# Kernel optimization log

Measured on AMD Instinct MI355X. Metric: run time of the kernel, lower is better.

## Reference

```python
import jax, jax.numpy as jnp
import numpy as np

EQUATION = "bik,bkj->bij"  # matches init_kwargs


def setup_inputs() -> dict:
    key = jax.random.key(0)
    k0, k1 = jax.random.split(key)
    B, I, K, J = 32, 2048, 128, 2048
    input_0 = jax.random.normal(k0, (B, I, K), dtype=jnp.float32)
    input_1 = jax.random.normal(k1, (B, K, J), dtype=jnp.float32)
    return {"input_0": input_0, "input_1": input_1}


def reference(input_0, input_1):
    # Einsum module forward: binary contraction per the stored equation,
    # alpha=1, beta=0 (defaults in EinsumFunction when kwargs is empty).
    return jnp.einsum(EQUATION, input_0, input_1)
```

## Files before the change

kernel.cpp:

```cpp
#include <hip/hip_runtime.h>
#include <hip/hip_bf16.h>
#include <stdint.h>

#define B_DIM 32
#define I_DIM 2048
#define J_DIM 2048
#define K_DIM 128

typedef __attribute__((ext_vector_type(8))) short bf16x8;
typedef __attribute__((ext_vector_type(4))) short short4v;
typedef __attribute__((ext_vector_type(4))) float f32x4;

__device__ inline short f2bf(float f) {
  union { float f; uint32_t u; } v; v.f = f;
  uint32_t u = v.u + 0x7fffu + ((v.u >> 16) & 1u);
  return (short)(u >> 16);
}

__global__ __launch_bounds__(256) void convA_kernel(const float* __restrict__ A,
                                                    short* __restrict__ Ab) {
  const int idx = blockIdx.x * 256 + threadIdx.x;
  const float4* p = reinterpret_cast<const float4*>(A) + (size_t)idx * 2;
  const float4 a = p[0], b = p[1];
  bf16x8 o;
  o[0] = f2bf(a.x); o[1] = f2bf(a.y); o[2] = f2bf(a.z); o[3] = f2bf(a.w);
  o[4] = f2bf(b.x); o[5] = f2bf(b.y); o[6] = f2bf(b.z); o[7] = f2bf(b.w);
  reinterpret_cast<bf16x8*>(Ab)[idx] = o;
}

__global__ __launch_bounds__(256) void transB_kernel(const float* __restrict__ B,
                                                     short* __restrict__ Bt) {
  __shared__ __align__(16) short tile[64 * 128];
  const int t  = threadIdx.x;
  const int j0 = blockIdx.x * 64;
  const int b  = blockIdx.y;
  const float* Bb = B + (size_t)b * K_DIM * J_DIM;
  const int jj = t & 63, kq = t >> 6;
  #pragma unroll
  for (int kr = 0; kr < 32; ++kr) {
    const int k = kr * 4 + kq;
    const float v = Bb[(size_t)k * J_DIM + j0 + jj];
    tile[jj * 128 + (k ^ ((jj & 15) << 3))] = f2bf(v);
  }
  __syncthreads();
  short* Btb = Bt + (size_t)b * J_DIM * K_DIM;
  const int slot = t & 15, jr = t >> 4;
  #pragma unroll
  for (int r2 = 0; r2 < 4; ++r2) {
    const int j  = r2 * 16 + jr;
    const bf16x8 v = *reinterpret_cast<const bf16x8*>(&tile[j * 128 + slot * 8]);
    const int k0 = (slot * 8) ^ ((j & 15) << 3);
    *reinterpret_cast<bf16x8*>(Btb + (size_t)(j0 + j) * K_DIM + k0) = v;
  }
}

#define GLD_LDS16(g, l) __builtin_amdgcn_global_load_lds( \
    (const __attribute__((address_space(1))) uint32_t*)(g), \
    (__attribute__((address_space(3))) uint32_t*)(l), 16, 0, 0)

__global__ __launch_bounds__(256, 4) void gemm_kernel(const short* __restrict__ Ab,
                                                      const short* __restrict__ Bt,
                                                      float* __restrict__ C) {
  __shared__ __align__(16) short As[8192];
  __shared__ __align__(16) short Bs[8192];
  const int t  = threadIdx.x;
  const int jt = blockIdx.x, it = blockIdx.y, b = blockIdx.z;

  const int rsub  = t >> 3;
  const int kbyte = ((t & 7) << 4) ^ ((rsub & 7) << 4);
  const char* Asrc = (const char*)(Ab + (size_t)(b * I_DIM + it * 128 + rsub) * K_DIM) + kbyte;
  const char* Bsrc = (const char*)(Bt + (size_t)(b * J_DIM + jt * 128 + rsub) * K_DIM) + kbyte;
  char* Adst = (char*)As + (t >> 6) * 1024;
  char* Bdst = (char*)Bs + (t >> 6) * 1024;

  const int w = t >> 6, wm = w >> 1, wn = w & 1;
  const int lane = t & 63, lr = lane & 15, g = lane >> 4;
  const int swr = (lr & 7) << 4;

  f32x4 acc[4][4];
  #pragma unroll
  for (int m = 0; m < 4; ++m)
    #pragma unroll
    for (int n = 0; n < 4; ++n)
      acc[m][n] = (f32x4){0.f, 0.f, 0.f, 0.f};

  #pragma unroll
  for (int ki = 0; ki < 2; ++ki) {
    if (ki) __syncthreads();
    #pragma unroll
    for (int q = 0; q < 4; ++q) {
      GLD_LDS16(Asrc + q * 8192 + ki * 128, Adst + q * 4096);
      GLD_LDS16(Bsrc + q * 8192 + ki * 128, Bdst + q * 4096);
    }
    __syncthreads();
    #pragma unroll
    for (int kk = 0; kk < 2; ++kk) {
      bf16x8 af[4], bb[4];
      const int cb = kk * 64 + g * 16;
      #pragma unroll
      for (int m = 0; m < 4; ++m) {
        const int R = wm * 64 + m * 16 + lr;
        af[m] = *reinterpret_cast<const bf16x8*>((const char*)As + R * 128 + (cb ^ swr));
      }
      #pragma unroll
      for (int n = 0; n < 4; ++n) {
        const int R = wn * 64 + n * 16 + lr;
        bb[n] = *reinterpret_cast<const bf16x8*>((const char*)Bs + R * 128 + (cb ^ swr));
      }
      #pragma unroll
      for (int m = 0; m < 4; ++m)
        #pragma unroll
        for (int n = 0; n < 4; ++n)
          acc[m][n] = __builtin_amdgcn_mfma_f32_16x16x32_bf16(af[m], bb[n], acc[m][n], 0, 0, 0);
    }
  }

  float* Cb = C + (size_t)b * I_DIM * J_DIM;
  const int cbase = jt * 128 + wn * 64 + lr;
  #pragma unroll
  for (int m = 0; m < 4; ++m) {
    const int rbase = it * 128 + wm * 64 + m * 16 + g * 4;
    #pragma unroll
    for (int q = 0; q < 4; ++q) {
      float* crow = Cb + (size_t)(rbase + q) * J_DIM + cbase;
      #pragma unroll
      for (int n = 0; n < 4; ++n) crow[n * 16] = acc[m][n][q];
    }
  }
}

__device__ inline int swz_fb(int row, int kbyte) {
  return row * 128 + ((kbyte ^ ((row & 15) << 4)) >> 1);
}

__global__ __launch_bounds__(256, 2) void bmm_fallback(const float* __restrict__ A,
                                                       const float* __restrict__ Bm,
                                                       float* __restrict__ C) {
  __shared__ short As[128 * 128];
  __shared__ short Bs[128 * 128];
  const int t  = threadIdx.x;
  const int jt = blockIdx.x, it = blockIdx.y, b = blockIdx.z;
  const float* Abp = A  + (size_t)b * I_DIM * K_DIM;
  const float* Bbp = Bm + (size_t)b * K_DIM * J_DIM;
  {
    const int r0 = t >> 5;
    const int k0 = (t & 31) * 4;
    #pragma unroll 4
    for (int i8 = 0; i8 < 16; ++i8) {
      const int r = i8 * 8 + r0;
      const float4 v = *reinterpret_cast<const float4*>(
          Abp + (size_t)(it * 128 + r) * K_DIM + k0);
      short4v s; s.x = f2bf(v.x); s.y = f2bf(v.y); s.z = f2bf(v.z); s.w = f2bf(v.w);
      *reinterpret_cast<short4v*>(&As[swz_fb(r, 2 * k0)]) = s;
    }
  }
  {
    const int j  = t & 127;
    const int kq = (t >> 7) * 4;
    #pragma unroll 4
    for (int kb = 0; kb < 16; ++kb) {
      const int k0 = kb * 8 + kq;
      const float* p = Bbp + (size_t)k0 * J_DIM + jt * 128 + j;
      const float f0 = p[0], f1 = p[J_DIM], f2 = p[2 * J_DIM], f3 = p[3 * J_DIM];
      short4v s; s.x = f2bf(f0); s.y = f2bf(f1); s.z = f2bf(f2); s.w = f2bf(f3);
      *reinterpret_cast<short4v*>(&Bs[swz_fb(j, 2 * k0)]) = s;
    }
  }
  __syncthreads();
  const int w = t >> 6, wm = w >> 1, wn = w & 1;
  const int lane = t & 63, lr = lane & 15, g = lane >> 4;
  f32x4 acc[4][4];
  #pragma unroll
  for (int m = 0; m < 4; ++m)
    #pragma unroll
    for (int n = 0; n < 4; ++n) acc[m][n] = (f32x4){0.f, 0.f, 0.f, 0.f};
  #pragma unroll
  for (int kk = 0; kk < 4; ++kk) {
    bf16x8 af[4], bfr[4];
    const int kb = kk * 64 + g * 16;
    #pragma unroll
    for (int m = 0; m < 4; ++m) {
      const int r = wm * 64 + m * 16 + lr;
      af[m] = *reinterpret_cast<const bf16x8*>(&As[swz_fb(r, kb)]);
    }
    #pragma unroll
    for (int n = 0; n < 4; ++n) {
      const int r = wn * 64 + n * 16 + lr;
      bfr[n] = *reinterpret_cast<const bf16x8*>(&Bs[swz_fb(r, kb)]);
    }
    #pragma unroll
    for (int m = 0; m < 4; ++m)
      #pragma unroll
      for (int n = 0; n < 4; ++n)
        acc[m][n] = __builtin_amdgcn_mfma_f32_16x16x32_bf16(af[m], bfr[n], acc[m][n], 0, 0, 0);
  }
  float* Cb = C + (size_t)b * I_DIM * J_DIM;
  const int cbase = jt * 128 + wn * 64 + lr;
  #pragma unroll
  for (int m = 0; m < 4; ++m) {
    const int rbase = it * 128 + wm * 64 + m * 16 + g * 4;
    #pragma unroll
    for (int q = 0; q < 4; ++q) {
      float* crow = Cb + (size_t)(rbase + q) * J_DIM + cbase;
      #pragma unroll
      for (int n = 0; n < 4; ++n) crow[n * 16] = acc[m][n][q];
    }
  }
}

extern "C" void kernel_launch(void* const* d_in, const int* in_sizes, int n_in,
                              void* d_out, int out_size, void* d_ws, size_t ws_size,
                              hipStream_t stream) {
  const float* A  = (const float*)d_in[0];
  const float* Bm = (const float*)d_in[1];
  float* C = (float*)d_out;
  const size_t needA = (size_t)B_DIM * I_DIM * K_DIM * sizeof(short);
  const size_t needB = (size_t)B_DIM * K_DIM * J_DIM * sizeof(short);
  if (ws_size >= needA + needB) {
    short* Ab = (short*)d_ws;
    short* Bt = (short*)((char*)d_ws + needA);
    convA_kernel<<<4096, 256, 0, stream>>>(A, Ab);
    transB_kernel<<<dim3(J_DIM / 64, B_DIM), 256, 0, stream>>>(Bm, Bt);
    gemm_kernel<<<dim3(J_DIM / 128, I_DIM / 128, B_DIM), 256, 0, stream>>>(Ab, Bt, C);
  } else {
    bmm_fallback<<<dim3(J_DIM / 128, I_DIM / 128, B_DIM), 256, 0, stream>>>(A, Bm, C);
  }
}
```

Measured before the change: 147.7 us.

## Restructure GEMM into single-wave 64x64 tiles with barrier-free LDS prefetch

Replaces the 256-thread 128x128 tile GEMM with a 64-thread, single-wavefront kernel that computes a 64x64 tile. Because only one wave uses the LDS, workgroup barriers are replaced by explicit waitcnt and sched_barrier fencing. The second K-half is loaded into the same LDS buffer once the first half's fragments are in registers, so it overlaps the remaining MFMAs. A 1D grid with a blockIdx remap interleaves batches and tiles across dispatch. The cost is less data reuse per tile, which roughly doubles global and LDS reads of A and B per output element, plus many more small workgroups.

```diff
diff --git a/kernel.cpp b/kernel.cpp
--- a/kernel.cpp
+++ b/kernel.cpp
@@ -58,24 +58,24 @@
     (const __attribute__((address_space(1))) uint32_t*)(g), \
     (__attribute__((address_space(3))) uint32_t*)(l), 16, 0, 0)
 
-__global__ __launch_bounds__(256, 4) void gemm_kernel(const short* __restrict__ Ab,
-                                                      const short* __restrict__ Bt,
-                                                      float* __restrict__ C) {
-  __shared__ __align__(16) short As[8192];
-  __shared__ __align__(16) short Bs[8192];
-  const int t  = threadIdx.x;
-  const int jt = blockIdx.x, it = blockIdx.y, b = blockIdx.z;
-
-  const int rsub  = t >> 3;
-  const int kbyte = ((t & 7) << 4) ^ ((rsub & 7) << 4);
-  const char* Asrc = (const char*)(Ab + (size_t)(b * I_DIM + it * 128 + rsub) * K_DIM) + kbyte;
-  const char* Bsrc = (const char*)(Bt + (size_t)(b * J_DIM + jt * 128 + rsub) * K_DIM) + kbyte;
-  char* Adst = (char*)As + (t >> 6) * 1024;
-  char* Bdst = (char*)Bs + (t >> 6) * 1024;
-
-  const int w = t >> 6, wm = w >> 1, wn = w & 1;
-  const int lane = t & 63, lr = lane & 15, g = lane >> 4;
-  const int swr = (lr & 7) << 4;
+__global__ __launch_bounds__(64, 4) void gemm_kernel(const short* __restrict__ Ab,
+                                                     const short* __restrict__ Bt,
+                                                     float* __restrict__ C) {
+  __shared__ __align__(16) char lds[16384];
+  const int l = threadIdx.x;
+
+  const int p   = blockIdx.x;
+  const int lid = ((p & 7) << 12) | (p >> 3);
+  const int jt  = lid & 31;
+  const int it  = (lid >> 5) & 31;
+  const int b   = lid >> 10;
+
+  const int rs = l >> 3;
+  const int cs = ((l & 7) ^ rs) << 4;
+  const char* Ag = (const char*)(Ab + ((size_t)b * I_DIM + it * 64 + rs) * K_DIM) + cs;
+  const char* Bg = (const char*)(Bt + ((size_t)b * J_DIM + jt * 64 + rs) * K_DIM) + cs;
+
+  const int lr = l & 15, g = l >> 4;
 
   f32x4 acc[4][4];
   #pragma unroll
@@ -85,41 +85,59 @@
       acc[m][n] = (f32x4){0.f, 0.f, 0.f, 0.f};
 
   #pragma unroll
-  for (int ki = 0; ki < 2; ++ki) {
-    if (ki) __syncthreads();
-    #pragma unroll
-    for (int q = 0; q < 4; ++q) {
-      GLD_LDS16(Asrc + q * 8192 + ki * 128, Adst + q * 4096);
-      GLD_LDS16(Bsrc + q * 8192 + ki * 128, Bdst + q * 4096);
-    }
-    __syncthreads();
-    #pragma unroll
-    for (int kk = 0; kk < 2; ++kk) {
-      bf16x8 af[4], bb[4];
-      const int cb = kk * 64 + g * 16;
-      #pragma unroll
-      for (int m = 0; m < 4; ++m) {
-        const int R = wm * 64 + m * 16 + lr;
-        af[m] = *reinterpret_cast<const bf16x8*>((const char*)As + R * 128 + (cb ^ swr));
+  for (int i = 0; i < 8; ++i) {
+    GLD_LDS16(Ag + i * 2048, lds + i * 1024);
+    GLD_LDS16(Bg + i * 2048, lds + 8192 + i * 1024);
+  }
+  asm volatile("s_waitcnt vmcnt(0)" ::: "memory");
+  __builtin_amdgcn_sched_barrier(0);
+
+  #pragma unroll
+  for (int ph = 0; ph < 2; ++ph) {
+    bf16x8 af[4], bf[4];
+    #pragma unroll
+    for (int m = 0; m < 4; ++m) {
+      const int R = m * 16 + lr;
+      af[m] = *reinterpret_cast<const bf16x8*>(lds + R * 128 + ((g ^ (lr & 7)) << 4));
+      bf[m] = *reinterpret_cast<const bf16x8*>(lds + 8192 + R * 128 + ((g ^ (lr & 7)) << 4));
+    }
+    #pragma unroll
+    for (int m = 0; m < 4; ++m)
+      #pragma unroll
+      for (int n = 0; n < 4; ++n)
+        acc[m][n] = __builtin_amdgcn_mfma_f32_16x16x32_bf16(af[m], bf[n], acc[m][n], 0, 0, 0);
+    #pragma unroll
+    for (int m = 0; m < 4; ++m) {
+      const int R = m * 16 + lr;
+      af[m] = *reinterpret_cast<const bf16x8*>(lds + R * 128 + (((4 | g) ^ (lr & 7)) << 4));
+      bf[m] = *reinterpret_cast<const bf16x8*>(lds + 8192 + R * 128 + (((4 | g) ^ (lr & 7)) << 4));
+    }
+    if (ph == 0) {
+      asm volatile("s_waitcnt lgkmcnt(0)" ::: "memory");
+      __builtin_amdgcn_sched_barrier(0);
+      #pragma unroll
+      for (int i = 0; i < 8; ++i) {
+        GLD_LDS16(Ag + i * 2048 + 128, lds + i * 1024);
+        GLD_LDS16(Bg + i * 2048 + 128, lds + 8192 + i * 1024);
       }
-      #pragma unroll
-      for (int n = 0; n < 4; ++n) {
-        const int R = wn * 64 + n * 16 + lr;
-        bb[n] = *reinterpret_cast<const bf16x8*>((const char*)Bs + R * 128 + (cb ^ swr));
-      }
-      #pragma unroll
-      for (int m = 0; m < 4; ++m)
-        #pragma unroll
-        for (int n = 0; n < 4; ++n)
-          acc[m][n] = __builtin_amdgcn_mfma_f32_16x16x32_bf16(af[m], bb[n], acc[m][n], 0, 0, 0);
+      __builtin_amdgcn_sched_barrier(0);
+    }
+    #pragma unroll
+    for (int m = 0; m < 4; ++m)
+      #pragma unroll
+      for (int n = 0; n < 4; ++n)
+        acc[m][n] = __builtin_amdgcn_mfma_f32_16x16x32_bf16(af[m], bf[n], acc[m][n], 0, 0, 0);
+    if (ph == 0) {
+      asm volatile("s_waitcnt vmcnt(0)" ::: "memory");
+      __builtin_amdgcn_sched_barrier(0);
     }
   }
 
   float* Cb = C + (size_t)b * I_DIM * J_DIM;
-  const int cbase = jt * 128 + wn * 64 + lr;
+  const int cbase = jt * 64 + lr;
   #pragma unroll
   for (int m = 0; m < 4; ++m) {
-    const int rbase = it * 128 + wm * 64 + m * 16 + g * 4;
+    const int rbase = it * 64 + m * 16 + g * 4;
     #pragma unroll
     for (int q = 0; q < 4; ++q) {
       float* crow = Cb + (size_t)(rbase + q) * J_DIM + cbase;
@@ -221,7 +239,7 @@
     short* Bt = (short*)((char*)d_ws + needA);
     convA_kernel<<<4096, 256, 0, stream>>>(A, Ab);
     transB_kernel<<<dim3(J_DIM / 64, B_DIM), 256, 0, stream>>>(Bm, Bt);
-    gemm_kernel<<<dim3(J_DIM / 128, I_DIM / 128, B_DIM), 256, 0, stream>>>(Ab, Bt, C);
+    gemm_kernel<<<32768, 64, 0, stream>>>(Ab, Bt, C);
   } else {
     bmm_fallback<<<dim3(J_DIM / 128, I_DIM / 128, B_DIM), 256, 0, stream>>>(A, Bm, C);
   }
```

New measurement: 176.5 us. 19.5% more time.

## Reuse A tile across four J tiles and overlap B reload with C stores

Applied to the files above, without the earlier changes.

The GEMM kernel becomes a flattened 2048-block grid. Each block loads its full-K A tile once into LDS and loops over four consecutive J tiles. After each tile's MFMAs it issues the next B tile's global-to-LDS load before writing C, so the load overlaps the output stores. This cuts redundant A traffic and block count, but doubles LDS per block (occupancy hint drops to 2). The vmcnt(63) wait depends on in-order counter semantics with many outstanding stores, which risks a race on the B buffer.

```diff
diff --git a/kernel.cpp b/kernel.cpp
--- a/kernel.cpp
+++ b/kernel.cpp
@@ -58,54 +58,63 @@
     (const __attribute__((address_space(1))) uint32_t*)(g), \
     (__attribute__((address_space(3))) uint32_t*)(l), 16, 0, 0)
 
-__global__ __launch_bounds__(256, 4) void gemm_kernel(const short* __restrict__ Ab,
+__global__ __launch_bounds__(256, 2) void gemm_kernel(const short* __restrict__ Ab,
                                                       const short* __restrict__ Bt,
                                                       float* __restrict__ C) {
-  __shared__ __align__(16) short As[8192];
-  __shared__ __align__(16) short Bs[8192];
-  const int t  = threadIdx.x;
-  const int jt = blockIdx.x, it = blockIdx.y, b = blockIdx.z;
-
-  const int rsub  = t >> 3;
-  const int kbyte = ((t & 7) << 4) ^ ((rsub & 7) << 4);
-  const char* Asrc = (const char*)(Ab + (size_t)(b * I_DIM + it * 128 + rsub) * K_DIM) + kbyte;
-  const char* Bsrc = (const char*)(Bt + (size_t)(b * J_DIM + jt * 128 + rsub) * K_DIM) + kbyte;
-  char* Adst = (char*)As + (t >> 6) * 1024;
-  char* Bdst = (char*)Bs + (t >> 6) * 1024;
+  __shared__ __align__(16) short As[128 * 128];
+  __shared__ __align__(16) short Bs[128 * 128];
+  const int t = threadIdx.x;
+  const int p = blockIdx.x;
+  const int jg = p & 3, it = (p >> 2) & 15, b = p >> 6;
 
   const int w = t >> 6, wm = w >> 1, wn = w & 1;
   const int lane = t & 63, lr = lane & 15, g = lane >> 4;
-  const int swr = (lr & 7) << 4;
-
-  f32x4 acc[4][4];
-  #pragma unroll
-  for (int m = 0; m < 4; ++m)
-    #pragma unroll
-    for (int n = 0; n < 4; ++n)
-      acc[m][n] = (f32x4){0.f, 0.f, 0.f, 0.f};
-
-  #pragma unroll
-  for (int ki = 0; ki < 2; ++ki) {
-    if (ki) __syncthreads();
-    #pragma unroll
-    for (int q = 0; q < 4; ++q) {
-      GLD_LDS16(Asrc + q * 8192 + ki * 128, Adst + q * 4096);
-      GLD_LDS16(Bsrc + q * 8192 + ki * 128, Bdst + q * 4096);
-    }
-    __syncthreads();
-    #pragma unroll
-    for (int kk = 0; kk < 2; ++kk) {
+
+  const int srow  = t >> 4;
+  const int sbyte = ((t & 15) ^ srow) << 4;
+  const char* Asrc  = (const char*)(Ab + ((size_t)b * I_DIM + it * 128 + srow) * K_DIM) + sbyte;
+  const char* Bbase = (const char*)(Bt + ((size_t)b * J_DIM + srow) * K_DIM) + sbyte;
+  char* Adst = (char*)As + w * 1024;
+  char* Bdst = (char*)Bs + w * 1024;
+
+  #pragma unroll
+  for (int i = 0; i < 8; ++i) GLD_LDS16(Asrc + i * 4096, Adst + i * 4096);
+  {
+    const char* Bsrc = Bbase + (size_t)(jg * 4) * 128 * 256;
+    #pragma unroll
+    for (int i = 0; i < 8; ++i) GLD_LDS16(Bsrc + i * 4096, Bdst + i * 4096);
+  }
+  asm volatile("s_waitcnt vmcnt(0)" ::: "memory");
+  __builtin_amdgcn_sched_barrier(0);
+  __builtin_amdgcn_s_barrier();
+  __builtin_amdgcn_sched_barrier(0);
+
+  float* Cb = C + (size_t)b * I_DIM * J_DIM;
+
+  #pragma unroll
+  for (int q = 0; q < 4; ++q) {
+    const int jt = jg * 4 + q;
+
+    f32x4 acc[4][4];
+    #pragma unroll
+    for (int m = 0; m < 4; ++m)
+      #pragma unroll
+      for (int n = 0; n < 4; ++n)
+        acc[m][n] = (f32x4){0.f, 0.f, 0.f, 0.f};
+
+    #pragma unroll
+    for (int kg = 0; kg < 4; ++kg) {
+      const int sl = kg * 4 + g;
       bf16x8 af[4], bb[4];
-      const int cb = kk * 64 + g * 16;
       #pragma unroll
       for (int m = 0; m < 4; ++m) {
         const int R = wm * 64 + m * 16 + lr;
-        af[m] = *reinterpret_cast<const bf16x8*>((const char*)As + R * 128 + (cb ^ swr));
+        af[m] = *reinterpret_cast<const bf16x8*>((const char*)As + R * 256 + ((sl ^ lr) << 4));
       }
       #pragma unroll
       for (int n = 0; n < 4; ++n) {
         const int R = wn * 64 + n * 16 + lr;
-        bb[n] = *reinterpret_cast<const bf16x8*>((const char*)Bs + R * 128 + (cb ^ swr));
+        bb[n] = *reinterpret_cast<const bf16x8*>((const char*)Bs + R * 256 + ((sl ^ lr) << 4));
       }
       #pragma unroll
       for (int m = 0; m < 4; ++m)
@@ -113,18 +122,33 @@
         for (int n = 0; n < 4; ++n)
           acc[m][n] = __builtin_amdgcn_mfma_f32_16x16x32_bf16(af[m], bb[n], acc[m][n], 0, 0, 0);
     }
-  }
-
-  float* Cb = C + (size_t)b * I_DIM * J_DIM;
-  const int cbase = jt * 128 + wn * 64 + lr;
-  #pragma unroll
-  for (int m = 0; m < 4; ++m) {
-    const int rbase = it * 128 + wm * 64 + m * 16 + g * 4;
-    #pragma unroll
-    for (int q = 0; q < 4; ++q) {
-      float* crow = Cb + (size_t)(rbase + q) * J_DIM + cbase;
-      #pragma unroll
-      for (int n = 0; n < 4; ++n) crow[n * 16] = acc[m][n][q];
+
+    __builtin_amdgcn_s_barrier();
+    __builtin_amdgcn_sched_barrier(0);
+
+    if (q < 3) {
+      const char* Bsrc = Bbase + (size_t)(jt + 1) * 128 * 256;
+      #pragma unroll
+      for (int i = 0; i < 8; ++i) GLD_LDS16(Bsrc + i * 4096, Bdst + i * 4096);
+    }
+
+    const int cbase = jt * 128 + wn * 64 + lr;
+    #pragma unroll
+    for (int m = 0; m < 4; ++m) {
+      const int rbase = it * 128 + wm * 64 + m * 16 + g * 4;
+      #pragma unroll
+      for (int qq = 0; qq < 4; ++qq) {
+        float* crow = Cb + (size_t)(rbase + qq) * J_DIM + cbase;
+        #pragma unroll
+        for (int n = 0; n < 4; ++n) crow[n * 16] = acc[m][n][qq];
+      }
+    }
+
+    if (q < 3) {
+      asm volatile("s_waitcnt vmcnt(63)" ::: "memory");
+      __builtin_amdgcn_sched_barrier(0);
+      __builtin_amdgcn_s_barrier();
+      __builtin_amdgcn_sched_barrier(0);
     }
   }
 }
@@ -221,7 +245,7 @@
     short* Bt = (short*)((char*)d_ws + needA);
     convA_kernel<<<4096, 256, 0, stream>>>(A, Ab);
     transB_kernel<<<dim3(J_DIM / 64, B_DIM), 256, 0, stream>>>(Bm, Bt);
-    gemm_kernel<<<dim3(J_DIM / 128, I_DIM / 128, B_DIM), 256, 0, stream>>>(Ab, Bt, C);
+    gemm_kernel<<<2048, 256, 0, stream>>>(Ab, Bt, C);
   } else {
     bmm_fallback<<<dim3(J_DIM / 128, I_DIM / 128, B_DIM), 256, 0, stream>>>(A, Bm, C);
   }
```

After: 139.7 us. 1.06x faster.
